# Optimization experiments

Hardware: AMD Instinct MI355X
Metric: run time of the kernel (lower is better)

Reference implementation:

```python
import jax, jax.numpy as jnp
import numpy as np

V, E, H, S, B, L = 10000, 512, 1024, 64, 64, 2

def setup_inputs() -> dict:
    key = jax.random.key(0)
    ks = iter(jax.random.split(key, 32))
    k_emb = 0.1
    k_h = float(np.sqrt(1.0 / H))
    inp = {}
    inp['inputs'] = jax.random.randint(next(ks), (S, B), 0, V)
    inp['init_hidden'] = jnp.zeros((L, B, H), jnp.float32)
    inp['emb_table'] = jax.random.uniform(next(ks), (V, E), jnp.float32, -k_emb, k_emb)
    in_feats = [E + H, 2 * H]
    for l in range(L):
        fi = in_feats[l]
        for nm in ('Wr', 'Wz', 'Wh'):
            inp[f'{nm}{l}'] = jax.random.uniform(next(ks), (fi, H), jnp.float32, -k_h, k_h)
        for nm in ('br', 'bz', 'bh'):
            inp[f'{nm}{l}'] = jax.random.uniform(next(ks), (H,), jnp.float32, -k_h, k_h)
    inp['Wfc0'] = jax.random.uniform(next(ks), (H, H), jnp.float32, -k_h, k_h)
    inp['bfc0'] = jax.random.uniform(next(ks), (H,), jnp.float32, -k_h, k_h)
    inp['Wout'] = jax.random.uniform(next(ks), (H, V), jnp.float32, -0.1, 0.1)
    inp['bout'] = jnp.zeros((V,), jnp.float32)
    return inp

def reference(inputs, init_hidden, emb_table,
              Wr0, Wz0, Wh0, br0, bz0, bh0,
              Wr1, Wz1, Wh1, br1, bz1, bh1,
              Wfc0, bfc0, Wout, bout):
    layers = [(Wr0, br0, Wz0, bz0, Wh0, bh0), (Wr1, br1, Wz1, bz1, Wh1, bh1)]
    fcs = [(Wfc0, bfc0)]
    emb = emb_table[inputs]  # [S, B, E]

    def step(h_prev, xt):
        # h_prev: [L, B, H]; xt: [B, E]
        x = xt
        hs = []
        for l, (Wr, br, Wz, bz, Wh, bh) in enumerate(layers):
            h = h_prev[l]
            cat = jnp.concatenate([x, h], axis=1)
            r = jax.nn.sigmoid(cat @ Wr + br)
            z = jax.nn.sigmoid(cat @ Wz + bz)
            h_hat = jax.nn.sigmoid(jnp.concatenate([x, r * h], axis=1) @ Wh + bh)
            ht = (1.0 - z) * h + z * h_hat
            hs.append(ht)
            if l < len(layers) - 1:
                Wfc, bfc = fcs[l]
                x = jax.nn.sigmoid(ht @ Wfc + bfc)  # dropout identity (keep_prob=1)
        logits_t = hs[-1] @ Wout + bout  # [B, V]
        return jnp.stack(hs, axis=0), logits_t

    h_final, logits = jax.lax.scan(step, init_hidden, emb)
    return logits, h_final  # [S, B, V], [L, B, H]
```

## Files before the change

kernel.cpp:

```cpp
#include <hip/hip_runtime.h>
#include <hip/hip_bf16.h>

typedef __attribute__((ext_vector_type(8))) short short8;
typedef __attribute__((ext_vector_type(4))) float f32x4;

#define S_ 64
#define B_ 64
#define H_ 1024
#define E_ 512
#define V_ 10000
#define M_ 4096
#define VPAD 10048
#define NBLK 64

__device__ __forceinline__ float sigmoidf_(float x) {
  return 1.0f / (1.0f + __expf(-x));
}

__device__ __forceinline__ void gbar(int* flags, int* gen, int idx) {
  __syncthreads();
  if (blockIdx.x == 0) {
    if (threadIdx.x < 64) {
      int lane = threadIdx.x;
      if (lane == 0)
        __hip_atomic_store(&flags[0], idx, __ATOMIC_RELEASE, __HIP_MEMORY_SCOPE_AGENT);
      for (;;) {
        int v = __hip_atomic_load(&flags[lane], __ATOMIC_RELAXED, __HIP_MEMORY_SCOPE_AGENT);
        if (__all(v >= idx)) break;
        __builtin_amdgcn_s_sleep(1);
      }
      __builtin_amdgcn_fence(__ATOMIC_ACQUIRE, "agent");
      if (lane == 0)
        __hip_atomic_store(gen, idx, __ATOMIC_RELEASE, __HIP_MEMORY_SCOPE_AGENT);
    }
  } else {
    if (threadIdx.x == 0) {
      __hip_atomic_store(&flags[blockIdx.x], idx, __ATOMIC_RELEASE, __HIP_MEMORY_SCOPE_AGENT);
      while (__hip_atomic_load(gen, __ATOMIC_RELAXED, __HIP_MEMORY_SCOPE_AGENT) < idx)
        __builtin_amdgcn_s_sleep(1);
      __builtin_amdgcn_fence(__ATOMIC_ACQUIRE, "agent");
    }
  }
  __syncthreads();
}

__global__ void bias_concat(const float* br0, const float* bz0, const float* bh0,
                            const float* br1, const float* bz1, const float* bh1,
                            float* b0cat, float* b1cat) {
  int i = blockIdx.x * 256 + threadIdx.x;
  if (i >= 3072) return;
  if (i < 1024)       { b0cat[i] = br0[i];        b1cat[i] = br1[i]; }
  else if (i < 2048)  { b0cat[i] = bz0[i - 1024]; b1cat[i] = bz1[i - 1024]; }
  else                { b0cat[i] = bh0[i - 2048]; b1cat[i] = bh1[i - 2048]; }
}

__global__ void transpose_cast(const float* __restrict__ src, __hip_bfloat16* __restrict__ dst,
                               int R, int C) {
  __shared__ float tile[32][33];
  int c0 = blockIdx.x * 32, r0 = blockIdx.y * 32;
  int tx = threadIdx.x & 31, ty = threadIdx.x >> 5;
#pragma unroll
  for (int i = 0; i < 4; ++i) {
    int r = r0 + ty + i * 8;
    int c = c0 + tx;
    if (r < R && c < C) tile[ty + i * 8][tx] = src[(size_t)r * C + c];
  }
  __syncthreads();
#pragma unroll
  for (int i = 0; i < 4; ++i) {
    int c = c0 + ty + i * 8;
    int r = r0 + tx;
    if (c < C && r < R) dst[(size_t)c * R + r] = __float2bfloat16(tile[tx][ty + i * 8]);
  }
}

__global__ void embed_cast(const int* __restrict__ inputs, const float* __restrict__ emb,
                           __hip_bfloat16* __restrict__ X0) {
  int idx = blockIdx.x * 256 + threadIdx.x;
  int i = idx >> 7;
  int e4 = idx & 127;
  int tok = inputs[i];
  const float4* src = (const float4*)(emb + (size_t)tok * E_);
  float4 v = src[e4];
  __hip_bfloat16* dst = X0 + (size_t)i * E_ + e4 * 4;
  dst[0] = __float2bfloat16(v.x);
  dst[1] = __float2bfloat16(v.y);
  dst[2] = __float2bfloat16(v.z);
  dst[3] = __float2bfloat16(v.w);
}

__global__ __launch_bounds__(256) void gemm_bf16(
    const __hip_bfloat16* __restrict__ A, const __hip_bfloat16* __restrict__ BT,
    const float* __restrict__ bias, void* __restrict__ C,
    int M, int N, int K, int act, int out_bf16) {
  __shared__ unsigned short Al[64 * 72];
  __shared__ unsigned short Bl[64 * 72];
  const int m0 = blockIdx.y * 64, n0 = blockIdx.x * 64;
  const int tid = threadIdx.x;
  const int wave = tid >> 6, lane = tid & 63;
  const int quad = lane >> 4, lr = lane & 15;
  const int wm = (wave >> 1) * 32, wn = (wave & 1) * 32;
  const int srow = tid >> 2, scol = (tid & 3) << 4;

  f32x4 acc[2][2];
#pragma unroll
  for (int a = 0; a < 2; ++a)
#pragma unroll
    for (int b = 0; b < 2; ++b) acc[a][b] = (f32x4){0.f, 0.f, 0.f, 0.f};

  const __hip_bfloat16* Ag = A + (size_t)(m0 + srow) * K + scol;
  const __hip_bfloat16* Bg = BT + (size_t)(n0 + srow) * K + scol;

  for (int kb = 0; kb < K; kb += 64) {
    short8 a0 = *(const short8*)(Ag + kb);
    short8 a1 = *(const short8*)(Ag + kb + 8);
    short8 b0 = *(const short8*)(Bg + kb);
    short8 b1 = *(const short8*)(Bg + kb + 8);
    *(short8*)&Al[srow * 72 + scol] = a0;
    *(short8*)&Al[srow * 72 + scol + 8] = a1;
    *(short8*)&Bl[srow * 72 + scol] = b0;
    *(short8*)&Bl[srow * 72 + scol + 8] = b1;
    __syncthreads();
#pragma unroll
    for (int k2 = 0; k2 < 64; k2 += 32) {
      short8 af0 = *(const short8*)&Al[(wm + lr) * 72 + k2 + quad * 8];
      short8 af1 = *(const short8*)&Al[(wm + 16 + lr) * 72 + k2 + quad * 8];
      short8 bf0 = *(const short8*)&Bl[(wn + lr) * 72 + k2 + quad * 8];
      short8 bf1 = *(const short8*)&Bl[(wn + 16 + lr) * 72 + k2 + quad * 8];
      acc[0][0] = __builtin_amdgcn_mfma_f32_16x16x32_bf16(af0, bf0, acc[0][0], 0, 0, 0);
      acc[0][1] = __builtin_amdgcn_mfma_f32_16x16x32_bf16(af0, bf1, acc[0][1], 0, 0, 0);
      acc[1][0] = __builtin_amdgcn_mfma_f32_16x16x32_bf16(af1, bf0, acc[1][0], 0, 0, 0);
      acc[1][1] = __builtin_amdgcn_mfma_f32_16x16x32_bf16(af1, bf1, acc[1][1], 0, 0, 0);
    }
    __syncthreads();
  }

#pragma unroll
  for (int mi = 0; mi < 2; ++mi)
#pragma unroll
    for (int ni = 0; ni < 2; ++ni) {
      int n = n0 + wn + ni * 16 + lr;
      if (n >= N) continue;
      float bv = bias ? bias[n] : 0.f;
#pragma unroll
      for (int r = 0; r < 4; ++r) {
        int m = m0 + wm + mi * 16 + quad * 4 + r;
        float v = acc[mi][ni][r] + bv;
        if (act) v = sigmoidf_(v);
        if (out_bf16) ((__hip_bfloat16*)C)[(size_t)m * N + n] = __float2bfloat16(v);
        else          ((float*)C)[(size_t)m * N + n] = v;
      }
    }
}

__global__ __launch_bounds__(256, 1) void gru_recurrent(
    const float* __restrict__ G, const __hip_bfloat16* __restrict__ WT,
    const float* __restrict__ init_h,
    __hip_bfloat16* __restrict__ h_bf, __hip_bfloat16* __restrict__ rh_bf,
    __hip_bfloat16* __restrict__ Hseq, float* __restrict__ h_final,
    int* __restrict__ bar_flags, int* __restrict__ bar_gen) {
  __shared__ unsigned short Wl[48 * 1032];

  const int bid = blockIdx.x;
  const int tid = threadIdx.x;
  const int wave = tid >> 6, lane = tid & 63;
  const int quad = lane >> 4, lr = lane & 15;
  const int nb = bid * 16;

  for (int c = tid; c < 48 * 128; c += 256) {
    int row = c >> 7;
    int col16 = c & 127;
    int seg = row >> 4, srow = row & 15;
    short8 v = *(const short8*)(WT + (size_t)(seg * 1024 + nb + srow) * H_ + col16 * 8);
    *(short8*)&Wl[row * 1032 + col16 * 8] = v;
  }

  float hreg[4], zreg[4];
#pragma unroll
  for (int r = 0; r < 4; ++r) {
    int mm = wave * 16 + quad * 4 + r;
    float v = init_h[mm * H_ + nb + lr];
    hreg[r] = v;
    zreg[r] = 0.f;
    h_bf[mm * H_ + nb + lr] = __float2bfloat16(v);
  }
  int bidx = 1;
  gbar(bar_flags, bar_gen, bidx++);

  for (int t = 0; t < S_; ++t) {
    float g0[4], g1[4], gh[4];
#pragma unroll
    for (int r = 0; r < 4; ++r) {
      int mm = wave * 16 + quad * 4 + r;
      const float* gp = G + (size_t)(t * B_ + mm) * 3072 + nb + lr;
      g0[r] = gp[0];
      g1[r] = gp[1024];
      gh[r] = gp[2048];
    }

    {
      const int am = wave * 16 + lr;
      const __hip_bfloat16* ap = h_bf + (size_t)am * H_ + quad * 8;
      short8 areg[32];
#pragma unroll
      for (int kk = 0; kk < 32; ++kk) areg[kk] = *(const short8*)(ap + kk * 32);
      f32x4 acc0 = (f32x4){0.f, 0.f, 0.f, 0.f};
      f32x4 acc1 = (f32x4){0.f, 0.f, 0.f, 0.f};
#pragma unroll
      for (int kk = 0; kk < 32; ++kk) {
        short8 b0 = *(const short8*)&Wl[lr * 1032 + quad * 8 + kk * 32];
        short8 b1 = *(const short8*)&Wl[(16 + lr) * 1032 + quad * 8 + kk * 32];
        acc0 = __builtin_amdgcn_mfma_f32_16x16x32_bf16(areg[kk], b0, acc0, 0, 0, 0);
        acc1 = __builtin_amdgcn_mfma_f32_16x16x32_bf16(areg[kk], b1, acc1, 0, 0, 0);
      }
#pragma unroll
      for (int r = 0; r < 4; ++r) {
        int mm = wave * 16 + quad * 4 + r;
        float rv = sigmoidf_(acc0[r] + g0[r]);
        zreg[r] = sigmoidf_(acc1[r] + g1[r]);
        rh_bf[mm * H_ + nb + lr] = __float2bfloat16(rv * hreg[r]);
      }
    }
    gbar(bar_flags, bar_gen, bidx++);

    {
      const int am = wave * 16 + lr;
      const __hip_bfloat16* ap = rh_bf + (size_t)am * H_ + quad * 8;
      short8 areg[32];
#pragma unroll
      for (int kk = 0; kk < 32; ++kk) areg[kk] = *(const short8*)(ap + kk * 32);
      f32x4 acc = (f32x4){0.f, 0.f, 0.f, 0.f};
#pragma unroll
      for (int kk = 0; kk < 32; ++kk) {
        short8 b = *(const short8*)&Wl[(32 + lr) * 1032 + quad * 8 + kk * 32];
        acc = __builtin_amdgcn_mfma_f32_16x16x32_bf16(areg[kk], b, acc, 0, 0, 0);
      }
#pragma unroll
      for (int r = 0; r < 4; ++r) {
        int mm = wave * 16 + quad * 4 + r;
        int nn = nb + lr;
        float hh = sigmoidf_(acc[r] + gh[r]);
        float hn = hreg[r] + zreg[r] * (hh - hreg[r]);
        hreg[r] = hn;
        __hip_bfloat16 hb = __float2bfloat16(hn);
        h_bf[mm * H_ + nn] = hb;
        Hseq[(size_t)(t * B_ + mm) * H_ + nn] = hb;
        if (t == S_ - 1) h_final[mm * H_ + nn] = hn;
      }
    }
    gbar(bar_flags, bar_gen, bidx++);
  }
}

extern "C" void kernel_launch(void* const* d_in, const int* in_sizes, int n_in,
                              void* d_out, int out_size, void* d_ws, size_t ws_size,
                              hipStream_t stream) {
  const int*   inputs      = (const int*)d_in[0];
  const float* init_hidden = (const float*)d_in[1];
  const float* emb         = (const float*)d_in[2];
  const float* Wr0 = (const float*)d_in[3];
  const float* Wz0 = (const float*)d_in[4];
  const float* Wh0 = (const float*)d_in[5];
  const float* br0 = (const float*)d_in[6];
  const float* bz0 = (const float*)d_in[7];
  const float* bh0 = (const float*)d_in[8];
  const float* Wr1 = (const float*)d_in[9];
  const float* Wz1 = (const float*)d_in[10];
  const float* Wh1 = (const float*)d_in[11];
  const float* br1 = (const float*)d_in[12];
  const float* bz1 = (const float*)d_in[13];
  const float* bh1 = (const float*)d_in[14];
  const float* Wfc0 = (const float*)d_in[15];
  const float* bfc0 = (const float*)d_in[16];
  const float* Wout = (const float*)d_in[17];
  const float* bout = (const float*)d_in[18];
  float* out = (float*)d_out;

  char* ws = (char*)d_ws;
  size_t off = 0;
  auto alloc = [&](size_t bytes) -> char* {
    char* p = ws + off;
    off = (off + bytes + 255) & ~(size_t)255;
    return p;
  };
  int* bar = (int*)alloc(2048);
  __hip_bfloat16* W0xT  = (__hip_bfloat16*)alloc((size_t)3072 * E_ * 2);
  __hip_bfloat16* W0hT  = (__hip_bfloat16*)alloc((size_t)3072 * H_ * 2);
  __hip_bfloat16* WfcT  = (__hip_bfloat16*)alloc((size_t)H_ * H_ * 2);
  __hip_bfloat16* W1xT  = (__hip_bfloat16*)alloc((size_t)3072 * H_ * 2);
  __hip_bfloat16* W1hT  = (__hip_bfloat16*)alloc((size_t)3072 * H_ * 2);
  __hip_bfloat16* WoutT = (__hip_bfloat16*)alloc((size_t)VPAD * H_ * 2);
  float* b0cat = (float*)alloc(3072 * 4);
  float* b1cat = (float*)alloc(3072 * 4);
  __hip_bfloat16* X0    = (__hip_bfloat16*)alloc((size_t)M_ * E_ * 2);
  float* G              = (float*)alloc((size_t)M_ * 3072 * 4);
  __hip_bfloat16* Hseq0 = (__hip_bfloat16*)alloc((size_t)M_ * H_ * 2);
  __hip_bfloat16* X1    = (__hip_bfloat16*)alloc((size_t)M_ * H_ * 2);
  __hip_bfloat16* Hseq1 = (__hip_bfloat16*)alloc((size_t)M_ * H_ * 2);
  __hip_bfloat16* hb0 = (__hip_bfloat16*)alloc((size_t)B_ * H_ * 2);
  __hip_bfloat16* hb1 = (__hip_bfloat16*)alloc((size_t)B_ * H_ * 2);
  __hip_bfloat16* rh  = (__hip_bfloat16*)alloc((size_t)B_ * H_ * 2);
  (void)ws_size; (void)n_in; (void)in_sizes; (void)out_size;

  hipMemsetAsync(bar, 0, 2048, stream);

  hipLaunchKernelGGL(bias_concat, dim3(12), dim3(256), 0, stream,
                     br0, bz0, bh0, br1, bz1, bh1, b0cat, b1cat);

  auto tp = [&](const float* src, __hip_bfloat16* dst, int R, int C) {
    hipLaunchKernelGGL(transpose_cast, dim3((C + 31) / 32, (R + 31) / 32), dim3(256), 0,
                       stream, src, dst, R, C);
  };
  tp(Wr0,            W0xT,                E_, H_);
  tp(Wz0,            W0xT + 1024 * E_,    E_, H_);
  tp(Wh0,            W0xT + 2048 * E_,    E_, H_);
  tp(Wr0 + (size_t)E_ * H_, W0hT,               H_, H_);
  tp(Wz0 + (size_t)E_ * H_, W0hT + 1024 * H_,   H_, H_);
  tp(Wh0 + (size_t)E_ * H_, W0hT + 2048 * H_,   H_, H_);
  tp(Wfc0, WfcT, H_, H_);
  tp(Wr1,            W1xT,                H_, H_);
  tp(Wz1,            W1xT + 1024 * H_,    H_, H_);
  tp(Wh1,            W1xT + 2048 * H_,    H_, H_);
  tp(Wr1 + (size_t)H_ * H_, W1hT,               H_, H_);
  tp(Wz1 + (size_t)H_ * H_, W1hT + 1024 * H_,   H_, H_);
  tp(Wh1 + (size_t)H_ * H_, W1hT + 2048 * H_,   H_, H_);
  tp(Wout, WoutT, H_, V_);

  hipLaunchKernelGGL(embed_cast, dim3(M_ * (E_ / 4) / 256), dim3(256), 0, stream,
                     inputs, emb, X0);

  hipLaunchKernelGGL(gemm_bf16, dim3(3072 / 64, M_ / 64), dim3(256), 0, stream,
                     X0, W0xT, b0cat, (void*)G, M_, 3072, E_, 0, 0);

  {
    const float* Gp = G; const __hip_bfloat16* WTp = W0hT;
    const float* inith = init_hidden;
    __hip_bfloat16* hbp = hb0; __hip_bfloat16* rhp = rh;
    __hip_bfloat16* Hsp = Hseq0;
    float* hfin = out + (size_t)M_ * V_;
    int* f0 = bar; int* g0 = bar + 64;
    void* kargs[] = {(void*)&Gp, (void*)&WTp, (void*)&inith, (void*)&hbp,
                     (void*)&rhp, (void*)&Hsp, (void*)&hfin,
                     (void*)&f0, (void*)&g0};
    hipLaunchCooperativeKernel((const void*)gru_recurrent, dim3(NBLK), dim3(256),
                               kargs, 0, stream);
  }

  hipLaunchKernelGGL(gemm_bf16, dim3(H_ / 64, M_ / 64), dim3(256), 0, stream,
                     Hseq0, WfcT, bfc0, (void*)X1, M_, H_, H_, 1, 1);

  hipLaunchKernelGGL(gemm_bf16, dim3(3072 / 64, M_ / 64), dim3(256), 0, stream,
                     X1, W1xT, b1cat, (void*)G, M_, 3072, H_, 0, 0);

  {
    const float* Gp = G; const __hip_bfloat16* WTp = W1hT;
    const float* inith = init_hidden + (size_t)B_ * H_;
    __hip_bfloat16* hbp = hb1; __hip_bfloat16* rhp = rh;
    __hip_bfloat16* Hsp = Hseq1;
    float* hfin = out + (size_t)M_ * V_ + (size_t)B_ * H_;
    int* f1 = bar + 128; int* g1 = bar + 192;
    void* kargs[] = {(void*)&Gp, (void*)&WTp, (void*)&inith, (void*)&hbp,
                     (void*)&rhp, (void*)&Hsp, (void*)&hfin,
                     (void*)&f1, (void*)&g1};
    hipLaunchCooperativeKernel((const void*)gru_recurrent, dim3(NBLK), dim3(256),
                               kargs, 0, stream);
  }

  hipLaunchKernelGGL(gemm_bf16, dim3(VPAD / 64, M_ / 64), dim3(256), 0, stream,
                     Hseq1, WoutT, bout, (void*)out, M_, V_, H_, 0, 0);
}
```

Before: 2.611 ms.

## Fuse both GRU layers and FC into one wavefront-pipelined cooperative kernel

```diff
diff --git a/kernel.cpp b/kernel.cpp
--- a/kernel.cpp
+++ b/kernel.cpp
@@ -11,7 +11,7 @@
 #define V_ 10000
 #define M_ 4096
 #define VPAD 10048
-#define NBLK 64
+#define NBLK 256
 
 __device__ __forceinline__ float sigmoidf_(float x) {
   return 1.0f / (1.0f + __expf(-x));
@@ -25,8 +25,12 @@
       if (lane == 0)
         __hip_atomic_store(&flags[0], idx, __ATOMIC_RELEASE, __HIP_MEMORY_SCOPE_AGENT);
       for (;;) {
-        int v = __hip_atomic_load(&flags[lane], __ATOMIC_RELAXED, __HIP_MEMORY_SCOPE_AGENT);
-        if (__all(v >= idx)) break;
+        int v0 = __hip_atomic_load(&flags[lane],       __ATOMIC_RELAXED, __HIP_MEMORY_SCOPE_AGENT);
+        int v1 = __hip_atomic_load(&flags[lane + 64],  __ATOMIC_RELAXED, __HIP_MEMORY_SCOPE_AGENT);
+        int v2 = __hip_atomic_load(&flags[lane + 128], __ATOMIC_RELAXED, __HIP_MEMORY_SCOPE_AGENT);
+        int v3 = __hip_atomic_load(&flags[lane + 192], __ATOMIC_RELAXED, __HIP_MEMORY_SCOPE_AGENT);
+        int mn = min(min(v0, v1), min(v2, v3));
+        if (__all(mn >= idx)) break;
         __builtin_amdgcn_s_sleep(1);
       }
       __builtin_amdgcn_fence(__ATOMIC_ACQUIRE, "agent");
@@ -153,99 +157,244 @@
     }
 }
 
-__global__ __launch_bounds__(256, 1) void gru_recurrent(
-    const float* __restrict__ G, const __hip_bfloat16* __restrict__ WT,
+__global__ __launch_bounds__(256, 1) void gru_fused(
+    const float* __restrict__ G0,
+    const __hip_bfloat16* __restrict__ W0hT, const __hip_bfloat16* __restrict__ WfcT,
+    const __hip_bfloat16* __restrict__ W1xT, const __hip_bfloat16* __restrict__ W1hT,
+    const float* __restrict__ bfc, const float* __restrict__ b1cat,
     const float* __restrict__ init_h,
-    __hip_bfloat16* __restrict__ h_bf, __hip_bfloat16* __restrict__ rh_bf,
-    __hip_bfloat16* __restrict__ Hseq, float* __restrict__ h_final,
+    __hip_bfloat16* __restrict__ h0b, __hip_bfloat16* __restrict__ rh0,
+    __hip_bfloat16* __restrict__ h1b, __hip_bfloat16* __restrict__ rh1,
+    __hip_bfloat16* __restrict__ x1b, float* __restrict__ g1buf,
+    __hip_bfloat16* __restrict__ Hseq1, float* __restrict__ hfin,
     int* __restrict__ bar_flags, int* __restrict__ bar_gen) {
   __shared__ unsigned short Wl[48 * 1032];
 
   const int bid = blockIdx.x;
+  const int gang = bid >> 6;
+  const int gid = bid & 63;
   const int tid = threadIdx.x;
   const int wave = tid >> 6, lane = tid & 63;
   const int quad = lane >> 4, lr = lane & 15;
-  const int nb = bid * 16;
-
-  for (int c = tid; c < 48 * 128; c += 256) {
-    int row = c >> 7;
-    int col16 = c & 127;
-    int seg = row >> 4, srow = row & 15;
-    short8 v = *(const short8*)(WT + (size_t)(seg * 1024 + nb + srow) * H_ + col16 * 8);
-    *(short8*)&Wl[row * 1032 + col16 * 8] = v;
-  }
-
-  float hreg[4], zreg[4];
-#pragma unroll
-  for (int r = 0; r < 4; ++r) {
-    int mm = wave * 16 + quad * 4 + r;
-    float v = init_h[mm * H_ + nb + lr];
-    hreg[r] = v;
-    zreg[r] = 0.f;
-    h_bf[mm * H_ + nb + lr] = __float2bfloat16(v);
-  }
+
+  if (gang == 0 || gang == 3) {
+    const __hip_bfloat16* WT = (gang == 0) ? W0hT : W1hT;
+    const int nb = gid * 16;
+    for (int c = tid; c < 48 * 128; c += 256) {
+      int row = c >> 7, col = c & 127;
+      int seg = row >> 4, srow = row & 15;
+      short8 v = *(const short8*)(WT + (size_t)(seg * 1024 + nb + srow) * H_ + col * 8);
+      *(short8*)&Wl[row * 1032 + col * 8] = v;
+    }
+  } else if (gang == 1) {
+    const int nb = gid * 16;
+    for (int c = tid; c < 16 * 128; c += 256) {
+      int row = c >> 7, col = c & 127;
+      short8 v = *(const short8*)(WfcT + (size_t)(nb + row) * H_ + col * 8);
+      *(short8*)&Wl[row * 1032 + col * 8] = v;
+    }
+  } else {
+    const int nb = gid * 48;
+    for (int c = tid; c < 48 * 128; c += 256) {
+      int row = c >> 7, col = c & 127;
+      short8 v = *(const short8*)(W1xT + (size_t)(nb + row) * H_ + col * 8);
+      *(short8*)&Wl[row * 1032 + col * 8] = v;
+    }
+  }
+
+  float hreg[4], zreg[4], ghp[4];
+  float bias0 = 0.f, bias1 = 0.f, bias2 = 0.f;
+  if (gang == 0 || gang == 3) {
+    const float* ih = init_h + (gang == 3 ? B_ * H_ : 0);
+    __hip_bfloat16* hb = (gang == 0) ? h0b : h1b;
+    const int nb = gid * 16;
+#pragma unroll
+    for (int r = 0; r < 4; ++r) {
+      int mm = wave * 16 + quad * 4 + r;
+      float v = ih[mm * H_ + nb + lr];
+      hreg[r] = v; zreg[r] = 0.f; ghp[r] = 0.f;
+      hb[mm * H_ + nb + lr] = __float2bfloat16(v);
+    }
+  } else if (gang == 1) {
+    bias0 = bfc[gid * 16 + lr];
+  } else {
+    const int nb = gid * 48;
+    bias0 = b1cat[nb + lr];
+    bias1 = b1cat[nb + 16 + lr];
+    bias2 = b1cat[nb + 32 + lr];
+  }
+
   int bidx = 1;
   gbar(bar_flags, bar_gen, bidx++);
 
-  for (int t = 0; t < S_; ++t) {
-    float g0[4], g1[4], gh[4];
-#pragma unroll
-    for (int r = 0; r < 4; ++r) {
-      int mm = wave * 16 + quad * 4 + r;
-      const float* gp = G + (size_t)(t * B_ + mm) * 3072 + nb + lr;
-      g0[r] = gp[0];
-      g1[r] = gp[1024];
-      gh[r] = gp[2048];
-    }
-
-    {
-      const int am = wave * 16 + lr;
-      const __hip_bfloat16* ap = h_bf + (size_t)am * H_ + quad * 8;
-      short8 areg[32];
-#pragma unroll
-      for (int kk = 0; kk < 32; ++kk) areg[kk] = *(const short8*)(ap + kk * 32);
-      f32x4 acc0 = (f32x4){0.f, 0.f, 0.f, 0.f};
-      f32x4 acc1 = (f32x4){0.f, 0.f, 0.f, 0.f};
-#pragma unroll
-      for (int kk = 0; kk < 32; ++kk) {
-        short8 b0 = *(const short8*)&Wl[lr * 1032 + quad * 8 + kk * 32];
-        short8 b1 = *(const short8*)&Wl[(16 + lr) * 1032 + quad * 8 + kk * 32];
-        acc0 = __builtin_amdgcn_mfma_f32_16x16x32_bf16(areg[kk], b0, acc0, 0, 0, 0);
-        acc1 = __builtin_amdgcn_mfma_f32_16x16x32_bf16(areg[kk], b1, acc1, 0, 0, 0);
+  for (int k = 0; k < 132; ++k) {
+    if (gang == 0) {
+      if (k < 128) {
+        const int nb = gid * 16;
+        const int am = wave * 16 + lr;
+        const int t = k >> 1;
+        if (!(k & 1)) {
+          float g0v[4], g1v[4];
+#pragma unroll
+          for (int r = 0; r < 4; ++r) {
+            int mm = wave * 16 + quad * 4 + r;
+            const float* gp = G0 + (size_t)(t * B_ + mm) * 3072 + nb + lr;
+            g0v[r] = gp[0]; g1v[r] = gp[1024]; ghp[r] = gp[2048];
+          }
+          const __hip_bfloat16* ap = h0b + (size_t)am * H_ + quad * 8;
+          short8 areg[32];
+#pragma unroll
+          for (int kk = 0; kk < 32; ++kk) areg[kk] = *(const short8*)(ap + kk * 32);
+          f32x4 acc0 = (f32x4){0.f, 0.f, 0.f, 0.f};
+          f32x4 acc1 = (f32x4){0.f, 0.f, 0.f, 0.f};
+#pragma unroll
+          for (int kk = 0; kk < 32; ++kk) {
+            short8 b0 = *(const short8*)&Wl[lr * 1032 + quad * 8 + kk * 32];
+            short8 b1 = *(const short8*)&Wl[(16 + lr) * 1032 + quad * 8 + kk * 32];
+            acc0 = __builtin_amdgcn_mfma_f32_16x16x32_bf16(areg[kk], b0, acc0, 0, 0, 0);
+            acc1 = __builtin_amdgcn_mfma_f32_16x16x32_bf16(areg[kk], b1, acc1, 0, 0, 0);
+          }
+#pragma unroll
+          for (int r = 0; r < 4; ++r) {
+            int mm = wave * 16 + quad * 4 + r;
+            float rv = sigmoidf_(acc0[r] + g0v[r]);
+            zreg[r] = sigmoidf_(acc1[r] + g1v[r]);
+            rh0[mm * H_ + nb + lr] = __float2bfloat16(rv * hreg[r]);
+          }
+        } else {
+          const __hip_bfloat16* ap = rh0 + (size_t)am * H_ + quad * 8;
+          short8 areg[32];
+#pragma unroll
+          for (int kk = 0; kk < 32; ++kk) areg[kk] = *(const short8*)(ap + kk * 32);
+          f32x4 acc = (f32x4){0.f, 0.f, 0.f, 0.f};
+#pragma unroll
+          for (int kk = 0; kk < 32; ++kk) {
+            short8 b = *(const short8*)&Wl[(32 + lr) * 1032 + quad * 8 + kk * 32];
+            acc = __builtin_amdgcn_mfma_f32_16x16x32_bf16(areg[kk], b, acc, 0, 0, 0);
+          }
+#pragma unroll
+          for (int r = 0; r < 4; ++r) {
+            int mm = wave * 16 + quad * 4 + r;
+            int nn = nb + lr;
+            float hh = sigmoidf_(acc[r] + ghp[r]);
+            float hn = hreg[r] + zreg[r] * (hh - hreg[r]);
+            hreg[r] = hn;
+            h0b[mm * H_ + nn] = __float2bfloat16(hn);
+            if (t == S_ - 1) hfin[mm * H_ + nn] = hn;
+          }
+        }
       }
-#pragma unroll
-      for (int r = 0; r < 4; ++r) {
-        int mm = wave * 16 + quad * 4 + r;
-        float rv = sigmoidf_(acc0[r] + g0[r]);
-        zreg[r] = sigmoidf_(acc1[r] + g1[r]);
-        rh_bf[mm * H_ + nb + lr] = __float2bfloat16(rv * hreg[r]);
+    } else if (gang == 1) {
+      if (!(k & 1) && k >= 2 && k <= 128) {
+        const int nb = gid * 16;
+        const int am = wave * 16 + lr;
+        const __hip_bfloat16* ap = h0b + (size_t)am * H_ + quad * 8;
+        short8 areg[32];
+#pragma unroll
+        for (int kk = 0; kk < 32; ++kk) areg[kk] = *(const short8*)(ap + kk * 32);
+        f32x4 acc = (f32x4){0.f, 0.f, 0.f, 0.f};
+#pragma unroll
+        for (int kk = 0; kk < 32; ++kk) {
+          short8 b = *(const short8*)&Wl[lr * 1032 + quad * 8 + kk * 32];
+          acc = __builtin_amdgcn_mfma_f32_16x16x32_bf16(areg[kk], b, acc, 0, 0, 0);
+        }
+#pragma unroll
+        for (int r = 0; r < 4; ++r) {
+          int mm = wave * 16 + quad * 4 + r;
+          float v = sigmoidf_(acc[r] + bias0);
+          x1b[mm * H_ + nb + lr] = __float2bfloat16(v);
+        }
       }
-    }
-    gbar(bar_flags, bar_gen, bidx++);
-
-    {
-      const int am = wave * 16 + lr;
-      const __hip_bfloat16* ap = rh_bf + (size_t)am * H_ + quad * 8;
-      short8 areg[32];
-#pragma unroll
-      for (int kk = 0; kk < 32; ++kk) areg[kk] = *(const short8*)(ap + kk * 32);
-      f32x4 acc = (f32x4){0.f, 0.f, 0.f, 0.f};
-#pragma unroll
-      for (int kk = 0; kk < 32; ++kk) {
-        short8 b = *(const short8*)&Wl[(32 + lr) * 1032 + quad * 8 + kk * 32];
-        acc = __builtin_amdgcn_mfma_f32_16x16x32_bf16(areg[kk], b, acc, 0, 0, 0);
+    } else if (gang == 2) {
+      if ((k & 1) && k >= 3 && k <= 129) {
+        const int nb = gid * 48;
+        const int am = wave * 16 + lr;
+        const __hip_bfloat16* ap = x1b + (size_t)am * H_ + quad * 8;
+        short8 areg[32];
+#pragma unroll
+        for (int kk = 0; kk < 32; ++kk) areg[kk] = *(const short8*)(ap + kk * 32);
+        f32x4 a0 = (f32x4){0.f, 0.f, 0.f, 0.f};
+        f32x4 a1 = (f32x4){0.f, 0.f, 0.f, 0.f};
+        f32x4 a2 = (f32x4){0.f, 0.f, 0.f, 0.f};
+#pragma unroll
+        for (int kk = 0; kk < 32; ++kk) {
+          short8 b0 = *(const short8*)&Wl[lr * 1032 + quad * 8 + kk * 32];
+          short8 b1 = *(const short8*)&Wl[(16 + lr) * 1032 + quad * 8 + kk * 32];
+          short8 b2 = *(const short8*)&Wl[(32 + lr) * 1032 + quad * 8 + kk * 32];
+          a0 = __builtin_amdgcn_mfma_f32_16x16x32_bf16(areg[kk], b0, a0, 0, 0, 0);
+          a1 = __builtin_amdgcn_mfma_f32_16x16x32_bf16(areg[kk], b1, a1, 0, 0, 0);
+          a2 = __builtin_amdgcn_mfma_f32_16x16x32_bf16(areg[kk], b2, a2, 0, 0, 0);
+        }
+#pragma unroll
+        for (int r = 0; r < 4; ++r) {
+          int mm = wave * 16 + quad * 4 + r;
+          float* gp = g1buf + (size_t)mm * 3072 + nb + lr;
+          gp[0]  = a0[r] + bias0;
+          gp[16] = a1[r] + bias1;
+          gp[32] = a2[r] + bias2;
+        }
       }
-#pragma unroll
-      for (int r = 0; r < 4; ++r) {
-        int mm = wave * 16 + quad * 4 + r;
-        int nn = nb + lr;
-        float hh = sigmoidf_(acc[r] + gh[r]);
-        float hn = hreg[r] + zreg[r] * (hh - hreg[r]);
-        hreg[r] = hn;
-        __hip_bfloat16 hb = __float2bfloat16(hn);
-        h_bf[mm * H_ + nn] = hb;
-        Hseq[(size_t)(t * B_ + mm) * H_ + nn] = hb;
-        if (t == S_ - 1) h_final[mm * H_ + nn] = hn;
+    } else {
+      if (k >= 4) {
+        const int nb = gid * 16;
+        const int am = wave * 16 + lr;
+        if (!(k & 1)) {
+          if (k <= 130) {
+            float g0v[4], g1v[4];
+#pragma unroll
+            for (int r = 0; r < 4; ++r) {
+              int mm = wave * 16 + quad * 4 + r;
+              const float* gp = g1buf + (size_t)mm * 3072 + nb + lr;
+              g0v[r] = gp[0]; g1v[r] = gp[1024]; ghp[r] = gp[2048];
+            }
+            const __hip_bfloat16* ap = h1b + (size_t)am * H_ + quad * 8;
+            short8 areg[32];
+#pragma unroll
+            for (int kk = 0; kk < 32; ++kk) areg[kk] = *(const short8*)(ap + kk * 32);
+            f32x4 acc0 = (f32x4){0.f, 0.f, 0.f, 0.f};
+            f32x4 acc1 = (f32x4){0.f, 0.f, 0.f, 0.f};
+#pragma unroll
+            for (int kk = 0; kk < 32; ++kk) {
+              short8 b0 = *(const short8*)&Wl[lr * 1032 + quad * 8 + kk * 32];
+              short8 b1 = *(const short8*)&Wl[(16 + lr) * 1032 + quad * 8 + kk * 32];
+              acc0 = __builtin_amdgcn_mfma_f32_16x16x32_bf16(areg[kk], b0, acc0, 0, 0, 0);
+              acc1 = __builtin_amdgcn_mfma_f32_16x16x32_bf16(areg[kk], b1, acc1, 0, 0, 0);
+            }
+#pragma unroll
+            for (int r = 0; r < 4; ++r) {
+              int mm = wave * 16 + quad * 4 + r;
+              float rv = sigmoidf_(acc0[r] + g0v[r]);
+              zreg[r] = sigmoidf_(acc1[r] + g1v[r]);
+              rh1[mm * H_ + nb + lr] = __float2bfloat16(rv * hreg[r]);
+            }
+          }
+        } else {
+          if (k <= 131) {
+            const int t = (k - 5) >> 1;
+            const __hip_bfloat16* ap = rh1 + (size_t)am * H_ + quad * 8;
+            short8 areg[32];
+#pragma unroll
+            for (int kk = 0; kk < 32; ++kk) areg[kk] = *(const short8*)(ap + kk * 32);
+            f32x4 acc = (f32x4){0.f, 0.f, 0.f, 0.f};
+#pragma unroll
+            for (int kk = 0; kk < 32; ++kk) {
+              short8 b = *(const short8*)&Wl[(32 + lr) * 1032 + quad * 8 + kk * 32];
+              acc = __builtin_amdgcn_mfma_f32_16x16x32_bf16(areg[kk], b, acc, 0, 0, 0);
+            }
+#pragma unroll
+            for (int r = 0; r < 4; ++r) {
+              int mm = wave * 16 + quad * 4 + r;
+              int nn = nb + lr;
+              float hh = sigmoidf_(acc[r] + ghp[r]);
+              float hn = hreg[r] + zreg[r] * (hh - hreg[r]);
+              hreg[r] = hn;
+              __hip_bfloat16 hb = __float2bfloat16(hn);
+              h1b[mm * H_ + nn] = hb;
+              Hseq1[(size_t)(t * B_ + mm) * H_ + nn] = hb;
+              if (t == S_ - 1) hfin[B_ * H_ + mm * H_ + nn] = hn;
+            }
+          }
+        }
       }
     }
     gbar(bar_flags, bar_gen, bidx++);
@@ -294,12 +443,13 @@
   float* b1cat = (float*)alloc(3072 * 4);
   __hip_bfloat16* X0    = (__hip_bfloat16*)alloc((size_t)M_ * E_ * 2);
   float* G              = (float*)alloc((size_t)M_ * 3072 * 4);
-  __hip_bfloat16* Hseq0 = (__hip_bfloat16*)alloc((size_t)M_ * H_ * 2);
-  __hip_bfloat16* X1    = (__hip_bfloat16*)alloc((size_t)M_ * H_ * 2);
   __hip_bfloat16* Hseq1 = (__hip_bfloat16*)alloc((size_t)M_ * H_ * 2);
+  float* g1buf          = (float*)alloc((size_t)B_ * 3072 * 4);
+  __hip_bfloat16* x1b = (__hip_bfloat16*)alloc((size_t)B_ * H_ * 2);
   __hip_bfloat16* hb0 = (__hip_bfloat16*)alloc((size_t)B_ * H_ * 2);
   __hip_bfloat16* hb1 = (__hip_bfloat16*)alloc((size_t)B_ * H_ * 2);
-  __hip_bfloat16* rh  = (__hip_bfloat16*)alloc((size_t)B_ * H_ * 2);
+  __hip_bfloat16* rh0 = (__hip_bfloat16*)alloc((size_t)B_ * H_ * 2);
+  __hip_bfloat16* rh1 = (__hip_bfloat16*)alloc((size_t)B_ * H_ * 2);
   (void)ws_size; (void)n_in; (void)in_sizes; (void)out_size;
 
   hipMemsetAsync(bar, 0, 2048, stream);
@@ -333,36 +483,23 @@
                      X0, W0xT, b0cat, (void*)G, M_, 3072, E_, 0, 0);
 
   {
-    const float* Gp = G; const __hip_bfloat16* WTp = W0hT;
+    const float* Gp = G;
+    const __hip_bfloat16* w0h = W0hT; const __hip_bfloat16* wfc = WfcT;
+    const __hip_bfloat16* w1x = W1xT; const __hip_bfloat16* w1h = W1hT;
+    const float* bfcp = bfc0; const float* b1p = b1cat;
     const float* inith = init_hidden;
-    __hip_bfloat16* hbp = hb0; __hip_bfloat16* rhp = rh;
-    __hip_bfloat16* Hsp = Hseq0;
+    __hip_bfloat16* h0p = hb0; __hip_bfloat16* rh0p = rh0;
+    __hip_bfloat16* h1p = hb1; __hip_bfloat16* rh1p = rh1;
+    __hip_bfloat16* x1p = x1b; float* g1p = g1buf;
+    __hip_bfloat16* Hs1 = Hseq1;
     float* hfin = out + (size_t)M_ * V_;
-    int* f0 = bar; int* g0 = bar + 64;
-    void* kargs[] = {(void*)&Gp, (void*)&WTp, (void*)&inith, (void*)&hbp,
-                     (void*)&rhp, (void*)&Hsp, (void*)&hfin,
-                     (void*)&f0, (void*)&g0};
-    hipLaunchCooperativeKernel((const void*)gru_recurrent, dim3(NBLK), dim3(256),
-                               kargs, 0, stream);
-  }
-
-  hipLaunchKernelGGL(gemm_bf16, dim3(H_ / 64, M_ / 64), dim3(256), 0, stream,
-                     Hseq0, WfcT, bfc0, (void*)X1, M_, H_, H_, 1, 1);
-
-  hipLaunchKernelGGL(gemm_bf16, dim3(3072 / 64, M_ / 64), dim3(256), 0, stream,
-                     X1, W1xT, b1cat, (void*)G, M_, 3072, H_, 0, 0);
-
-  {
-    const float* Gp = G; const __hip_bfloat16* WTp = W1hT;
-    const float* inith = init_hidden + (size_t)B_ * H_;
-    __hip_bfloat16* hbp = hb1; __hip_bfloat16* rhp = rh;
-    __hip_bfloat16* Hsp = Hseq1;
-    float* hfin = out + (size_t)M_ * V_ + (size_t)B_ * H_;
-    int* f1 = bar + 128; int* g1 = bar + 192;
-    void* kargs[] = {(void*)&Gp, (void*)&WTp, (void*)&inith, (void*)&hbp,
-                     (void*)&rhp, (void*)&Hsp, (void*)&hfin,
-                     (void*)&f1, (void*)&g1};
-    hipLaunchCooperativeKernel((const void*)gru_recurrent, dim3(NBLK), dim3(256),
+    int* fl = bar; int* gn = bar + 256;
+    void* kargs[] = {(void*)&Gp, (void*)&w0h, (void*)&wfc, (void*)&w1x, (void*)&w1h,
+                     (void*)&bfcp, (void*)&b1p, (void*)&inith,
+                     (void*)&h0p, (void*)&rh0p, (void*)&h1p, (void*)&rh1p,
+                     (void*)&x1p, (void*)&g1p, (void*)&Hs1, (void*)&hfin,
+                     (void*)&fl, (void*)&gn};
+    hipLaunchCooperativeKernel((const void*)gru_fused, dim3(NBLK), dim3(256),
                                kargs, 0, stream);
   }
 
```

Result: faster. 2.525 ms (-3.3%).
